# Performance work log

Hardware: AMD Instinct MI355X
Metric: run time of the kernel (lower is better)

The kernel has to match this reference:

```python
import jax, jax.numpy as jnp
import numpy as np

B, S, H, E, F, TOP_K = 4, 2048, 512, 16, 1024, 2


def setup_inputs() -> dict:
    key = jax.random.key(0)
    k0, k1, k2, k3, k4 = jax.random.split(key, 5)
    scale = 0.02
    return {
        "inputs": jax.random.normal(k0, (B, S, H), dtype=jnp.float32),
        "router_w": jax.random.normal(k1, (E, H), dtype=jnp.float32) * scale,
        "gate_w": jax.random.normal(k2, (E, H, F), dtype=jnp.float32) * scale,
        "up_w": jax.random.normal(k3, (E, H, F), dtype=jnp.float32) * scale,
        "down_w": jax.random.normal(k4, (E, F, H), dtype=jnp.float32) * scale,
    }


def _moe_forward(inputs, router_w, gate_w, up_w, down_w):
    b, s, h = inputs.shape
    x = inputs.reshape(-1, h)                      # [T, H]
    T = x.shape[0]
    # --- routing: topk of logits then fp32 softmax over the k selected ---
    router_logits = x @ router_w.T                 # [T, E]
    top_vals, top_idx = jax.lax.top_k(router_logits, TOP_K)   # [T, K]
    weights = jax.nn.softmax(top_vals.astype(jnp.float32), axis=-1)  # [T, K]
    # dense combine weights: w[t, e] = routing weight if expert e selected else 0
    combine = jnp.zeros((T, router_w.shape[0]), jnp.float32)
    combine = combine.at[jnp.arange(T)[:, None], top_idx].set(weights)  # [T, E]

    # --- per-expert SwiGLU MLP, weighted combine (scan over experts) ---
    def step(acc, ew):
        wg, wu, wd, ce = ew                        # [H,F], [H,F], [F,H], [T]
        hid = jax.nn.silu(x @ wg) * (x @ wu)       # [T, F]
        y = hid @ wd                               # [T, H]
        return acc + ce[:, None] * y, None

    out0 = jnp.zeros_like(x)
    out, _ = jax.lax.scan(step, out0, (gate_w, up_w, down_w, combine.T))
    return out.reshape(b, s, h), router_logits, top_idx


def reference(inputs, router_w, gate_w, up_w, down_w):
    out, router_logits, selected_experts = _moe_forward(
        inputs, router_w, gate_w, up_w, down_w)
    return out
```

## Files before the change

kernel.cpp:

```cpp
#include <hip/hip_runtime.h>
#include <cstdint>
#include <cstddef>

#define T_TOK 8192
#define H_DIM 512
#define E_NUM 16
#define F_DIM 1024

typedef __bf16 bf16x8 __attribute__((ext_vector_type(8)));
typedef float f32x4 __attribute__((ext_vector_type(4)));

#define OFF_XBF  0UL
#define OFF_HID  8388608UL
#define OFF_GW   41943040UL
#define OFF_UW   58720256UL
#define OFF_DW   75497472UL
#define OFF_STOK 92274688UL
#define OFF_SW   92340224UL
#define OFF_TOPE 92405760UL
#define OFF_TOPW 92471296UL
#define OFF_CNT  92536832UL
#define OFF_CUR  92537856UL
#define OFF_OFFS 92538880UL
#define OFF_SIDX 92539904UL
#define OFF_L128 92605440UL
#define OFF_L64  92606464UL
#define OFF_YB   OFF_GW

__device__ __forceinline__ unsigned short f2bf(float f) {
  union { float f; uint32_t u; } v; v.f = f;
  uint32_t r = v.u + 0x7fffu + ((v.u >> 16) & 1u);
  return (unsigned short)(r >> 16);
}

__device__ __forceinline__ float bf2f(unsigned short u) {
  union { uint32_t u; float f; } v; v.u = (uint32_t)u << 16;
  return v.f;
}

__device__ __forceinline__ void gld16(const void* g, void* l) {
  __builtin_amdgcn_global_load_lds(
      (const __attribute__((address_space(1))) unsigned int*)g,
      (__attribute__((address_space(3))) unsigned int*)l, 16, 0, 0);
}

__device__ __forceinline__ uint4 pack8(const float4 v[8], int i) {
  uint4 q;
  q.x = (uint32_t)f2bf(((const float*)&v[0])[i]) | ((uint32_t)f2bf(((const float*)&v[1])[i]) << 16);
  q.y = (uint32_t)f2bf(((const float*)&v[2])[i]) | ((uint32_t)f2bf(((const float*)&v[3])[i]) << 16);
  q.z = (uint32_t)f2bf(((const float*)&v[4])[i]) | ((uint32_t)f2bf(((const float*)&v[5])[i]) << 16);
  q.w = (uint32_t)f2bf(((const float*)&v[6])[i]) | ((uint32_t)f2bf(((const float*)&v[7])[i]) << 16);
  return q;
}

__global__ __launch_bounds__(256) void k_pre(
    const float* __restrict__ x, const float* __restrict__ rw,
    const float* __restrict__ gw, const float* __restrict__ uw,
    unsigned short* __restrict__ xbf, int* __restrict__ tope,
    float* __restrict__ topw,
    unsigned short* __restrict__ gws, unsigned short* __restrict__ uws,
    int* __restrict__ counts) {
  const int bid = blockIdx.x;
  const int tid = threadIdx.x;
  __shared__ int lh[E_NUM];

  if (bid < 2048) {
    const int e = bid >> 7, mat = (bid >> 6) & 1, kc = (bid >> 2) & 15, f2 = bid & 3;
    const float* src = (mat ? uw : gw) + (size_t)e * H_DIM * F_DIM
                     + (size_t)kc * 32 * F_DIM + f2 * 256;
    unsigned short* dst = mat ? uws : gws;
    const int nb = tid & 63, kb = tid >> 6;
    const float* s0 = src + (size_t)kb * 8 * F_DIM + nb * 4;
    float4 v[8];
    #pragma unroll
    for (int j = 0; j < 8; ++j) v[j] = *(const float4*)(s0 + (size_t)j * F_DIM);
    #pragma unroll
    for (int i = 0; i < 4; ++i) {
      const int nl = nb * 4 + i;
      const int fx = f2 * 2 + (nl >> 7), fi = nl & 127;
      const size_t ob = (((size_t)e * 8 + fx) * 16 + kc) * 4096;
      *(uint4*)&dst[ob + fi * 32 + ((kb ^ fi) & 3) * 8] = pack8(v, i);
    }
  } else {
    if (tid < E_NUM) lh[tid] = 0;
    __syncthreads();
    const int rb = bid - 2048;
    const int wave = tid >> 6, lane = tid & 63;
    const int t = rb * 4 + wave;
    const float4* xr = (const float4*)(x + (size_t)t * H_DIM + lane * 8);
    float4 a = xr[0], b = xr[1];
    float xi[8] = {a.x, a.y, a.z, a.w, b.x, b.y, b.z, b.w};
    uint4 o;
    o.x = (uint32_t)f2bf(xi[0]) | ((uint32_t)f2bf(xi[1]) << 16);
    o.y = (uint32_t)f2bf(xi[2]) | ((uint32_t)f2bf(xi[3]) << 16);
    o.z = (uint32_t)f2bf(xi[4]) | ((uint32_t)f2bf(xi[5]) << 16);
    o.w = (uint32_t)f2bf(xi[6]) | ((uint32_t)f2bf(xi[7]) << 16);
    *(uint4*)(xbf + (size_t)t * H_DIM + lane * 8) = o;
    float acc[E_NUM];
    #pragma unroll
    for (int e = 0; e < E_NUM; ++e) {
      const float4* wr = (const float4*)(rw + e * H_DIM + lane * 8);
      float4 wa = wr[0], wb = wr[1];
      acc[e] = xi[0]*wa.x + xi[1]*wa.y + xi[2]*wa.z + xi[3]*wa.w
             + xi[4]*wb.x + xi[5]*wb.y + xi[6]*wb.z + xi[7]*wb.w;
    }
    #pragma unroll
    for (int off = 1; off < 64; off <<= 1) {
      #pragma unroll
      for (int e = 0; e < E_NUM; ++e) acc[e] += __shfl_xor(acc[e], off);
    }
    if (lane == 0) {
      int e0 = 0; float v0 = acc[0];
      #pragma unroll
      for (int e = 1; e < E_NUM; ++e) if (acc[e] > v0) { v0 = acc[e]; e0 = e; }
      int e1 = -1; float v1 = -3.4e38f;
      #pragma unroll
      for (int e = 0; e < E_NUM; ++e) if (e != e0 && acc[e] > v1) { v1 = acc[e]; e1 = e; }
      float ee = __expf(v1 - v0);
      float inv = 1.0f / (1.0f + ee);
      tope[t*2]   = e0; tope[t*2+1] = e1;
      topw[t*2]   = inv; topw[t*2+1] = ee * inv;
      atomicAdd(&lh[e0], 1);
      atomicAdd(&lh[e1], 1);
    }
    __syncthreads();
    if (tid < E_NUM && lh[tid] > 0) atomicAdd(&counts[tid * 16], lh[tid]);
  }
}

__global__ void k_offsets(const int* __restrict__ counts, int* __restrict__ offs,
                          int* __restrict__ list128, int* __restrict__ list64) {
  __shared__ int sc[16], b128[16], b64[16];
  if (threadIdx.x == 0) {
    int s = 0, a = 0, b = 0;
    for (int e = 0; e < E_NUM; ++e) {
      int c = counts[e * 16];
      sc[e] = c; b128[e] = a; b64[e] = b;
      offs[e] = s;
      s += c; a += (c + 127) >> 7; b += (c + 63) >> 6;
    }
    offs[16] = s; offs[18] = a; offs[19] = b;
  }
  __syncthreads();
  for (int e = 0; e < E_NUM; ++e) {
    const int n1 = (sc[e] + 127) >> 7;
    for (int ti = threadIdx.x; ti < n1; ti += 64) list128[b128[e] + ti] = (e << 24) | (ti << 7);
    const int n2 = (sc[e] + 63) >> 6;
    for (int ti = threadIdx.x; ti < n2; ti += 64) list64[b64[e] + ti] = (e << 24) | (ti << 6);
  }
}

__global__ __launch_bounds__(256) void k_scatter(
    const int* __restrict__ tope, const float* __restrict__ topw,
    const int* __restrict__ offs, int* __restrict__ cursors,
    int* __restrict__ stok, float* __restrict__ sw, int* __restrict__ sidx) {
  __shared__ int lh[E_NUM];
  __shared__ int lbase[E_NUM];
  const int tid = threadIdx.x;
  const int t = blockIdx.x * 256 + tid;
  if (tid < E_NUM) lh[tid] = 0;
  __syncthreads();
  int e0 = tope[t*2], e1 = tope[t*2+1];
  int r0 = atomicAdd(&lh[e0], 1);
  int r1 = atomicAdd(&lh[e1], 1);
  __syncthreads();
  if (tid < E_NUM) lbase[tid] = atomicAdd(&cursors[tid * 16], lh[tid]);
  __syncthreads();
  int s0 = offs[e0] + lbase[e0] + r0;
  int s1 = offs[e1] + lbase[e1] + r1;
  stok[s0] = t; sw[s0] = topw[t*2];
  stok[s1] = t; sw[s1] = topw[t*2+1];
  sidx[t*2] = s0; sidx[t*2+1] = s1;
}

__global__ __launch_bounds__(256, 2) void k_gateup(
    const unsigned short* __restrict__ xbf,
    const unsigned short* __restrict__ gws, const unsigned short* __restrict__ uws,
    const int* __restrict__ stok, const int* __restrict__ counts,
    const int* __restrict__ offs, const int* __restrict__ list128,
    unsigned short* __restrict__ hid,
    const float* __restrict__ dwf, unsigned short* __restrict__ dws) {
  const int y = blockIdx.y;
  const int tid = threadIdx.x;

  if (y >= 160) {
    const int u = (y - 160) * 8 + blockIdx.x;
    const int e = u >> 6, kc = (u >> 1) & 31, ht = u & 1;
    const float* src = dwf + (size_t)e * F_DIM * H_DIM
                     + (size_t)kc * 32 * H_DIM + ht * 256;
    const int nb = tid & 63, kb = tid >> 6;
    const float* s0 = src + (size_t)kb * 8 * H_DIM + nb * 4;
    float4 v[8];
    #pragma unroll
    for (int j = 0; j < 8; ++j) v[j] = *(const float4*)(s0 + (size_t)j * H_DIM);
    const size_t ob = (((size_t)e * 2 + ht) * 32 + kc) * 8192;
    #pragma unroll
    for (int i = 0; i < 4; ++i) {
      const int n = nb * 4 + i;
      *(uint4*)&dws[ob + n * 32 + ((kb ^ n) & 3) * 8] = pack8(v, i);
    }
    return;
  }
  if (y >= offs[18]) return;
  const int v = list128[y];
  const int e = v >> 24, t0 = v & 0xffffff;
  const int cnt = counts[e * 16];
  const int base = offs[e];
  const int fx = blockIdx.x;

  __shared__ __align__(16) unsigned short sb[2][3][4096];

  const int wave = tid >> 6, lane = tid & 63;
  const int l15 = lane & 15, hi = lane >> 4;
  const int wm = wave >> 1, wn = wave & 1;

  const int r0 = tid >> 2, slot = tid & 3;
  const int rr0 = min(t0 + r0, cnt - 1), rr1 = min(t0 + r0 + 64, cnt - 1);
  const char* sA0 = (const char*)xbf + (size_t)stok[base + rr0] * 1024 + ((slot ^ (r0 & 3)) * 16);
  const char* sA1 = (const char*)xbf + (size_t)stok[base + rr1] * 1024 + ((slot ^ (r0 & 3)) * 16);
  const char* sG = (const char*)gws + (((size_t)e * 8 + fx) * 16) * 8192 + tid * 16;
  const char* sU = (const char*)uws + (((size_t)e * 8 + fx) * 16) * 8192 + tid * 16;
  unsigned short* const dA = &sb[0][0][wave * 512];
  unsigned short* const dG = &sb[0][1][wave * 512];
  unsigned short* const dU = &sb[0][2][wave * 512];
  const int bufo = 3 * 4096;

  f32x4 accg[4][4] = {}; f32x4 accu[4][4] = {};

  #define STAGE_GU(b, kk) { \
    gld16(sA0 + (kk)*64, dA + (b)*bufo); \
    gld16(sA1 + (kk)*64, dA + (b)*bufo + 2048); \
    gld16(sG + (size_t)(kk)*8192, dG + (b)*bufo); \
    gld16(sG + (size_t)(kk)*8192 + 4096, dG + (b)*bufo + 2048); \
    gld16(sU + (size_t)(kk)*8192, dU + (b)*bufo); \
    gld16(sU + (size_t)(kk)*8192 + 4096, dU + (b)*bufo + 2048); }

  STAGE_GU(0, 0);
  __syncthreads();
  #pragma unroll 1
  for (int kk = 0; kk < 16; ++kk) {
    const int cur = kk & 1;
    if (kk < 15) STAGE_GU(cur ^ 1, kk + 1);
    const unsigned short* lA = &sb[cur][0][0];
    const unsigned short* lG = &sb[cur][1][0];
    const unsigned short* lU = &sb[cur][2][0];
    bf16x8 a[4], bg[4], bu[4];
    #pragma unroll
    for (int m = 0; m < 4; ++m) {
      int row = wm*64 + m*16 + l15;
      a[m] = *(const bf16x8*)((const char*)lA + row*64 + (((hi ^ row) & 3) << 4));
    }
    #pragma unroll
    for (int s = 0; s < 4; ++s) {
      int row = wn*64 + s*16 + l15;
      int o = row*64 + (((hi ^ row) & 3) << 4);
      bg[s] = *(const bf16x8*)((const char*)lG + o);
      bu[s] = *(const bf16x8*)((const char*)lU + o);
    }
    #pragma unroll
    for (int m = 0; m < 4; ++m)
      #pragma unroll
      for (int s = 0; s < 4; ++s) {
        accg[m][s] = __builtin_amdgcn_mfma_f32_16x16x32_bf16(a[m], bg[s], accg[m][s], 0, 0, 0);
        accu[m][s] = __builtin_amdgcn_mfma_f32_16x16x32_bf16(a[m], bu[s], accu[m][s], 0, 0, 0);
      }
    __syncthreads();
  }
  #undef STAGE_GU

  #pragma unroll
  for (int m = 0; m < 4; ++m)
    #pragma unroll
    for (int r = 0; r < 4; ++r) {
      int row = t0 + wm*64 + m*16 + hi*4 + r;
      if (row < cnt) {
        #pragma unroll
        for (int s = 0; s < 4; ++s) {
          float g = accg[m][s][r], u = accu[m][s][r];
          float h = g / (1.0f + __expf(-g)) * u;
          hid[(size_t)(base + row) * 1024 + fx*128 + wn*64 + s*16 + l15] = f2bf(h);
        }
      }
    }
}

__global__ __launch_bounds__(256, 3) void k_down(
    const unsigned short* __restrict__ hid, const unsigned short* __restrict__ dws,
    const int* __restrict__ counts, const int* __restrict__ offs,
    const int* __restrict__ list64, unsigned short* __restrict__ ybuf) {
  const int y = blockIdx.y;
  if (y >= offs[19]) return;
  const int v = list64[y];
  const int e = v >> 24, t0 = v & 0xffffff;
  const int cnt = counts[e * 16];
  const int base = offs[e];
  const int ht = blockIdx.x;

  __shared__ __align__(16) unsigned short sbA[2][2048];
  __shared__ __align__(16) unsigned short sbW[2][8192];

  const int tid = threadIdx.x;
  const int wave = tid >> 6, lane = tid & 63;
  const int l15 = lane & 15, hi = lane >> 4;

  const int r0 = tid >> 2, slot = tid & 3;
  const int rr = min(t0 + r0, cnt - 1);
  const char* sA = (const char*)hid + (size_t)(base + rr) * 2048 + ((slot ^ (r0 & 3)) * 16);
  const char* sW = (const char*)dws + (((size_t)e * 2 + ht) * 32) * 16384 + tid * 16;
  unsigned short* const dA = &sbA[0][wave * 512];
  unsigned short* const dW = &sbW[0][wave * 512];

  f32x4 acc[4][4] = {};

  #define STAGE_DN(b, kk) { \
    gld16(sA + (kk)*64, dA + (b)*2048); \
    const char* w = sW + (size_t)(kk)*16384; \
    gld16(w,         dW + (b)*8192); \
    gld16(w + 4096,  dW + (b)*8192 + 2048); \
    gld16(w + 8192,  dW + (b)*8192 + 4096); \
    gld16(w + 12288, dW + (b)*8192 + 6144); }

  STAGE_DN(0, 0);
  __syncthreads();
  #pragma unroll 1
  for (int kk = 0; kk < 32; ++kk) {
    const int cur = kk & 1;
    if (kk < 31) STAGE_DN(cur ^ 1, kk + 1);
    const unsigned short* lA = &sbA[cur][0];
    const unsigned short* lW = &sbW[cur][0];
    bf16x8 a[4], b[4];
    #pragma unroll
    for (int m = 0; m < 4; ++m) {
      int row = m*16 + l15;
      a[m] = *(const bf16x8*)((const char*)lA + row*64 + (((hi ^ row) & 3) << 4));
    }
    #pragma unroll
    for (int s = 0; s < 4; ++s) {
      int row = wave*64 + s*16 + l15;
      b[s] = *(const bf16x8*)((const char*)lW + row*64 + (((hi ^ row) & 3) << 4));
    }
    #pragma unroll
    for (int m = 0; m < 4; ++m)
      #pragma unroll
      for (int s = 0; s < 4; ++s)
        acc[m][s] = __builtin_amdgcn_mfma_f32_16x16x32_bf16(a[m], b[s], acc[m][s], 0, 0, 0);
    __syncthreads();
  }
  #undef STAGE_DN

  #pragma unroll
  for (int m = 0; m < 4; ++m)
    #pragma unroll
    for (int r = 0; r < 4; ++r) {
      int row = t0 + m*16 + hi*4 + r;
      if (row < cnt) {
        unsigned short* yy = ybuf + (size_t)(base + row) * 512 + ht*256 + wave*64;
        #pragma unroll
        for (int s = 0; s < 4; ++s)
          yy[s*16 + l15] = f2bf(acc[m][s][r]);
      }
    }
}

__global__ __launch_bounds__(256) void k_gather(
    const unsigned short* __restrict__ ybuf, const int* __restrict__ sidx,
    const float* __restrict__ topw, float* __restrict__ out) {
  const int wave = threadIdx.x >> 6, lane = threadIdx.x & 63;
  const int t = blockIdx.x * 4 + wave;
  const int s0 = sidx[t*2], s1 = sidx[t*2+1];
  const float w0 = topw[t*2], w1 = topw[t*2+1];
  uint4 a = *(const uint4*)(ybuf + (size_t)s0 * 512 + lane * 8);
  uint4 b = *(const uint4*)(ybuf + (size_t)s1 * 512 + lane * 8);
  float4 o0, o1;
  o0.x = w0*bf2f((unsigned short)(a.x)) + w1*bf2f((unsigned short)(b.x));
  o0.y = w0*bf2f((unsigned short)(a.x>>16)) + w1*bf2f((unsigned short)(b.x>>16));
  o0.z = w0*bf2f((unsigned short)(a.y)) + w1*bf2f((unsigned short)(b.y));
  o0.w = w0*bf2f((unsigned short)(a.y>>16)) + w1*bf2f((unsigned short)(b.y>>16));
  o1.x = w0*bf2f((unsigned short)(a.z)) + w1*bf2f((unsigned short)(b.z));
  o1.y = w0*bf2f((unsigned short)(a.z>>16)) + w1*bf2f((unsigned short)(b.z>>16));
  o1.z = w0*bf2f((unsigned short)(a.w)) + w1*bf2f((unsigned short)(b.w));
  o1.w = w0*bf2f((unsigned short)(a.w>>16)) + w1*bf2f((unsigned short)(b.w>>16));
  float* orow = out + (size_t)t * H_DIM + lane * 8;
  *(float4*)orow = o0;
  *(float4*)(orow + 4) = o1;
}

extern "C" void kernel_launch(void* const* d_in, const int* in_sizes, int n_in,
                              void* d_out, int out_size, void* d_ws, size_t ws_size,
                              hipStream_t stream) {
  const float* x  = (const float*)d_in[0];
  const float* rw = (const float*)d_in[1];
  const float* gw = (const float*)d_in[2];
  const float* uw = (const float*)d_in[3];
  const float* dw = (const float*)d_in[4];
  float* out = (float*)d_out;
  char* ws = (char*)d_ws;

  unsigned short* xbf = (unsigned short*)(ws + OFF_XBF);
  unsigned short* hid = (unsigned short*)(ws + OFF_HID);
  unsigned short* gws = (unsigned short*)(ws + OFF_GW);
  unsigned short* uws = (unsigned short*)(ws + OFF_UW);
  unsigned short* dws = (unsigned short*)(ws + OFF_DW);
  unsigned short* ybuf = (unsigned short*)(ws + OFF_YB);
  int*   stok    = (int*)(ws + OFF_STOK);
  float* swt     = (float*)(ws + OFF_SW);
  int*   tope    = (int*)(ws + OFF_TOPE);
  float* topw    = (float*)(ws + OFF_TOPW);
  int*   counts  = (int*)(ws + OFF_CNT);
  int*   cursors = (int*)(ws + OFF_CUR);
  int*   offs    = (int*)(ws + OFF_OFFS);
  int*   sidx    = (int*)(ws + OFF_SIDX);
  int*   list128 = (int*)(ws + OFF_L128);
  int*   list64  = (int*)(ws + OFF_L64);

  hipMemsetAsync(ws + OFF_CNT, 0, 2048 + 128, stream);

  k_pre<<<4096, 256, 0, stream>>>(x, rw, gw, uw, xbf, tope, topw, gws, uws, counts);
  k_offsets<<<1, 64, 0, stream>>>(counts, offs, list128, list64);
  k_scatter<<<T_TOK / 256, 256, 0, stream>>>(tope, topw, offs, cursors, stok, swt, sidx);
  k_gateup<<<dim3(8, 288), 256, 0, stream>>>(
      xbf, gws, uws, stok, counts, offs, list128, hid, dw, dws);
  k_down<<<dim3(2, 288), 256, 0, stream>>>(
      hid, dws, counts, offs, list64, ybuf);
  k_gather<<<T_TOK / 4, 256, 0, stream>>>(ybuf, sidx, topw, out);
}
```

Baseline: 157.3 us.

## Triple-buffer gate/up and down GEMM loads; move down-weight conversion to preprocessing kernel

Both grouped GEMM kernels move from double-buffered to triple-buffered LDS staging. They prefetch two k-steps ahead and use explicit vmcnt waits instead of __syncthreads, so global loads stay in flight across iterations. The down-weight fp32-to-bf16 conversion moves out of k_gateup into k_pre, which shrinks the gate/up grid. k_down's occupancy hint drops from 3 to 2 blocks per CU to make room for the larger shared memory, trading occupancy for deeper prefetch.

```diff
diff --git a/kernel.cpp b/kernel.cpp
--- a/kernel.cpp
+++ b/kernel.cpp
@@ -56,10 +56,11 @@
 __global__ __launch_bounds__(256) void k_pre(
     const float* __restrict__ x, const float* __restrict__ rw,
     const float* __restrict__ gw, const float* __restrict__ uw,
+    const float* __restrict__ dw,
     unsigned short* __restrict__ xbf, int* __restrict__ tope,
     float* __restrict__ topw,
     unsigned short* __restrict__ gws, unsigned short* __restrict__ uws,
-    int* __restrict__ counts) {
+    unsigned short* __restrict__ dws, int* __restrict__ counts) {
   const int bid = blockIdx.x;
   const int tid = threadIdx.x;
   __shared__ int lh[E_NUM];
@@ -81,10 +82,25 @@
       const size_t ob = (((size_t)e * 8 + fx) * 16 + kc) * 4096;
       *(uint4*)&dst[ob + fi * 32 + ((kb ^ fi) & 3) * 8] = pack8(v, i);
     }
+  } else if (bid < 3072) {
+    const int u = bid - 2048;
+    const int e = u >> 6, kc = (u >> 1) & 31, ht = u & 1;
+    const float* src = dw + (size_t)e * F_DIM * H_DIM + (size_t)kc * 32 * H_DIM + ht * 256;
+    const int nb = tid & 63, kb = tid >> 6;
+    const float* s0 = src + (size_t)kb * 8 * H_DIM + nb * 4;
+    float4 v[8];
+    #pragma unroll
+    for (int j = 0; j < 8; ++j) v[j] = *(const float4*)(s0 + (size_t)j * H_DIM);
+    const size_t ob = (((size_t)e * 2 + ht) * 32 + kc) * 8192;
+    #pragma unroll
+    for (int i = 0; i < 4; ++i) {
+      const int n = nb * 4 + i;
+      *(uint4*)&dws[ob + n * 32 + ((kb ^ n) & 3) * 8] = pack8(v, i);
+    }
   } else {
     if (tid < E_NUM) lh[tid] = 0;
     __syncthreads();
-    const int rb = bid - 2048;
+    const int rb = bid - 3072;
     const int wave = tid >> 6, lane = tid & 63;
     const int t = rb * 4 + wave;
     const float4* xr = (const float4*)(x + (size_t)t * H_DIM + lane * 8);
@@ -178,29 +194,8 @@
     const unsigned short* __restrict__ gws, const unsigned short* __restrict__ uws,
     const int* __restrict__ stok, const int* __restrict__ counts,
     const int* __restrict__ offs, const int* __restrict__ list128,
-    unsigned short* __restrict__ hid,
-    const float* __restrict__ dwf, unsigned short* __restrict__ dws) {
+    unsigned short* __restrict__ hid) {
   const int y = blockIdx.y;
-  const int tid = threadIdx.x;
-
-  if (y >= 160) {
-    const int u = (y - 160) * 8 + blockIdx.x;
-    const int e = u >> 6, kc = (u >> 1) & 31, ht = u & 1;
-    const float* src = dwf + (size_t)e * F_DIM * H_DIM
-                     + (size_t)kc * 32 * H_DIM + ht * 256;
-    const int nb = tid & 63, kb = tid >> 6;
-    const float* s0 = src + (size_t)kb * 8 * H_DIM + nb * 4;
-    float4 v[8];
-    #pragma unroll
-    for (int j = 0; j < 8; ++j) v[j] = *(const float4*)(s0 + (size_t)j * H_DIM);
-    const size_t ob = (((size_t)e * 2 + ht) * 32 + kc) * 8192;
-    #pragma unroll
-    for (int i = 0; i < 4; ++i) {
-      const int n = nb * 4 + i;
-      *(uint4*)&dws[ob + n * 32 + ((kb ^ n) & 3) * 8] = pack8(v, i);
-    }
-    return;
-  }
   if (y >= offs[18]) return;
   const int v = list128[y];
   const int e = v >> 24, t0 = v & 0xffffff;
@@ -208,8 +203,9 @@
   const int base = offs[e];
   const int fx = blockIdx.x;
 
-  __shared__ __align__(16) unsigned short sb[2][3][4096];
-
+  __shared__ __align__(16) unsigned short sb[3][3][4096];
+
+  const int tid = threadIdx.x;
   const int wave = tid >> 6, lane = tid & 63;
   const int l15 = lane & 15, hi = lane >> 4;
   const int wm = wave >> 1, wn = wave & 1;
@@ -235,37 +231,43 @@
     gld16(sU + (size_t)(kk)*8192, dU + (b)*bufo); \
     gld16(sU + (size_t)(kk)*8192 + 4096, dU + (b)*bufo + 2048); }
 
+  #define GU_CHUNK(kk, DO_STAGE, VM) { \
+    if (DO_STAGE) STAGE_GU(b2, (kk) + 2); \
+    asm volatile("s_waitcnt vmcnt(" VM ") lgkmcnt(0)\n\ts_barrier" ::: "memory"); \
+    const unsigned short* lA = &sb[b0][0][0]; \
+    const unsigned short* lG = &sb[b0][1][0]; \
+    const unsigned short* lU = &sb[b0][2][0]; \
+    bf16x8 a[4], bg[4], bu[4]; \
+    _Pragma("unroll") \
+    for (int m = 0; m < 4; ++m) { \
+      int row = wm*64 + m*16 + l15; \
+      a[m] = *(const bf16x8*)((const char*)lA + row*64 + (((hi ^ row) & 3) << 4)); \
+    } \
+    _Pragma("unroll") \
+    for (int s = 0; s < 4; ++s) { \
+      int row = wn*64 + s*16 + l15; \
+      int o = row*64 + (((hi ^ row) & 3) << 4); \
+      bg[s] = *(const bf16x8*)((const char*)lG + o); \
+      bu[s] = *(const bf16x8*)((const char*)lU + o); \
+    } \
+    _Pragma("unroll") \
+    for (int m = 0; m < 4; ++m) \
+      _Pragma("unroll") \
+      for (int s = 0; s < 4; ++s) { \
+        accg[m][s] = __builtin_amdgcn_mfma_f32_16x16x32_bf16(a[m], bg[s], accg[m][s], 0, 0, 0); \
+        accu[m][s] = __builtin_amdgcn_mfma_f32_16x16x32_bf16(a[m], bu[s], accu[m][s], 0, 0, 0); \
+      } \
+    asm volatile("s_waitcnt lgkmcnt(0)\n\ts_barrier" ::: "memory"); \
+    int _t = b0; b0 = b1; b1 = b2; b2 = _t; }
+
+  int b0 = 0, b1 = 1, b2 = 2;
   STAGE_GU(0, 0);
-  __syncthreads();
+  STAGE_GU(1, 1);
   #pragma unroll 1
-  for (int kk = 0; kk < 16; ++kk) {
-    const int cur = kk & 1;
-    if (kk < 15) STAGE_GU(cur ^ 1, kk + 1);
-    const unsigned short* lA = &sb[cur][0][0];
-    const unsigned short* lG = &sb[cur][1][0];
-    const unsigned short* lU = &sb[cur][2][0];
-    bf16x8 a[4], bg[4], bu[4];
-    #pragma unroll
-    for (int m = 0; m < 4; ++m) {
-      int row = wm*64 + m*16 + l15;
-      a[m] = *(const bf16x8*)((const char*)lA + row*64 + (((hi ^ row) & 3) << 4));
-    }
-    #pragma unroll
-    for (int s = 0; s < 4; ++s) {
-      int row = wn*64 + s*16 + l15;
-      int o = row*64 + (((hi ^ row) & 3) << 4);
-      bg[s] = *(const bf16x8*)((const char*)lG + o);
-      bu[s] = *(const bf16x8*)((const char*)lU + o);
-    }
-    #pragma unroll
-    for (int m = 0; m < 4; ++m)
-      #pragma unroll
-      for (int s = 0; s < 4; ++s) {
-        accg[m][s] = __builtin_amdgcn_mfma_f32_16x16x32_bf16(a[m], bg[s], accg[m][s], 0, 0, 0);
-        accu[m][s] = __builtin_amdgcn_mfma_f32_16x16x32_bf16(a[m], bu[s], accu[m][s], 0, 0, 0);
-      }
-    __syncthreads();
-  }
+  for (int kk = 0; kk < 14; ++kk) GU_CHUNK(kk, 1, "12");
+  GU_CHUNK(14, 0, "6");
+  GU_CHUNK(15, 0, "0");
+  #undef GU_CHUNK
   #undef STAGE_GU
 
   #pragma unroll
@@ -284,7 +286,7 @@
     }
 }
 
-__global__ __launch_bounds__(256, 3) void k_down(
+__global__ __launch_bounds__(256, 2) void k_down(
     const unsigned short* __restrict__ hid, const unsigned short* __restrict__ dws,
     const int* __restrict__ counts, const int* __restrict__ offs,
     const int* __restrict__ list64, unsigned short* __restrict__ ybuf) {
@@ -296,8 +298,8 @@
   const int base = offs[e];
   const int ht = blockIdx.x;
 
-  __shared__ __align__(16) unsigned short sbA[2][2048];
-  __shared__ __align__(16) unsigned short sbW[2][8192];
+  __shared__ __align__(16) unsigned short sbA[3][2048];
+  __shared__ __align__(16) unsigned short sbW[3][8192];
 
   const int tid = threadIdx.x;
   const int wave = tid >> 6, lane = tid & 63;
@@ -320,32 +322,38 @@
     gld16(w + 8192,  dW + (b)*8192 + 4096); \
     gld16(w + 12288, dW + (b)*8192 + 6144); }
 
+  #define DN_CHUNK(kk, DO_STAGE, VM) { \
+    if (DO_STAGE) STAGE_DN(b2, (kk) + 2); \
+    asm volatile("s_waitcnt vmcnt(" VM ") lgkmcnt(0)\n\ts_barrier" ::: "memory"); \
+    const unsigned short* lA = &sbA[b0][0]; \
+    const unsigned short* lW = &sbW[b0][0]; \
+    bf16x8 a[4], b[4]; \
+    _Pragma("unroll") \
+    for (int m = 0; m < 4; ++m) { \
+      int row = m*16 + l15; \
+      a[m] = *(const bf16x8*)((const char*)lA + row*64 + (((hi ^ row) & 3) << 4)); \
+    } \
+    _Pragma("unroll") \
+    for (int s = 0; s < 4; ++s) { \
+      int row = wave*64 + s*16 + l15; \
+      b[s] = *(const bf16x8*)((const char*)lW + row*64 + (((hi ^ row) & 3) << 4)); \
+    } \
+    _Pragma("unroll") \
+    for (int m = 0; m < 4; ++m) \
+      _Pragma("unroll") \
+      for (int s = 0; s < 4; ++s) \
+        acc[m][s] = __builtin_amdgcn_mfma_f32_16x16x32_bf16(a[m], b[s], acc[m][s], 0, 0, 0); \
+    asm volatile("s_waitcnt lgkmcnt(0)\n\ts_barrier" ::: "memory"); \
+    int _t = b0; b0 = b1; b1 = b2; b2 = _t; }
+
+  int b0 = 0, b1 = 1, b2 = 2;
   STAGE_DN(0, 0);
-  __syncthreads();
+  STAGE_DN(1, 1);
   #pragma unroll 1
-  for (int kk = 0; kk < 32; ++kk) {
-    const int cur = kk & 1;
-    if (kk < 31) STAGE_DN(cur ^ 1, kk + 1);
-    const unsigned short* lA = &sbA[cur][0];
-    const unsigned short* lW = &sbW[cur][0];
-    bf16x8 a[4], b[4];
-    #pragma unroll
-    for (int m = 0; m < 4; ++m) {
-      int row = m*16 + l15;
-      a[m] = *(const bf16x8*)((const char*)lA + row*64 + (((hi ^ row) & 3) << 4));
-    }
-    #pragma unroll
-    for (int s = 0; s < 4; ++s) {
-      int row = wave*64 + s*16 + l15;
-      b[s] = *(const bf16x8*)((const char*)lW + row*64 + (((hi ^ row) & 3) << 4));
-    }
-    #pragma unroll
-    for (int m = 0; m < 4; ++m)
-      #pragma unroll
-      for (int s = 0; s < 4; ++s)
-        acc[m][s] = __builtin_amdgcn_mfma_f32_16x16x32_bf16(a[m], b[s], acc[m][s], 0, 0, 0);
-    __syncthreads();
-  }
+  for (int kk = 0; kk < 30; ++kk) DN_CHUNK(kk, 1, "10");
+  DN_CHUNK(30, 0, "5");
+  DN_CHUNK(31, 0, "0");
+  #undef DN_CHUNK
   #undef STAGE_DN
 
   #pragma unroll
@@ -415,11 +423,11 @@
 
   hipMemsetAsync(ws + OFF_CNT, 0, 2048 + 128, stream);
 
-  k_pre<<<4096, 256, 0, stream>>>(x, rw, gw, uw, xbf, tope, topw, gws, uws, counts);
+  k_pre<<<5120, 256, 0, stream>>>(x, rw, gw, uw, dw, xbf, tope, topw, gws, uws, dws, counts);
   k_offsets<<<1, 64, 0, stream>>>(counts, offs, list128, list64);
   k_scatter<<<T_TOK / 256, 256, 0, stream>>>(tope, topw, offs, cursors, stok, swt, sidx);
-  k_gateup<<<dim3(8, 288), 256, 0, stream>>>(
-      xbf, gws, uws, stok, counts, offs, list128, hid, dw, dws);
+  k_gateup<<<dim3(8, 160), 256, 0, stream>>>(
+      xbf, gws, uws, stok, counts, offs, list128, hid);
   k_down<<<dim3(2, 288), 256, 0, stream>>>(
       hid, dws, counts, offs, list64, ybuf);
   k_gather<<<T_TOK / 4, 256, 0, stream>>>(ybuf, sidx, topw, out);
```

Result: slower. 174.7 us (+11.1%).

## Move down-weight conversion into pre kernel and raise occupancy bounds

Applied to the files above, without the earlier changes.

The fp32-to-bf16 conversion and swizzle of the down-projection weights moves out of the gate/up kernel's extra grid rows and into the pre kernel. Each conversion block now handles two column halves, which halves the block count for the gate/up and down weight conversion. The gate/up grid shrinks to the GEMM rows only, and the launch-bound occupancy hints rise to 3 for gate/up and 4 for down. The aim is less dead grid and fewer branches in the GEMM kernel, plus more waves per CU, at the cost of tighter register budgets that could cause spills.

```diff
diff --git a/kernel.cpp b/kernel.cpp
--- a/kernel.cpp
+++ b/kernel.cpp
@@ -56,35 +56,61 @@
 __global__ __launch_bounds__(256) void k_pre(
     const float* __restrict__ x, const float* __restrict__ rw,
     const float* __restrict__ gw, const float* __restrict__ uw,
+    const float* __restrict__ dw,
     unsigned short* __restrict__ xbf, int* __restrict__ tope,
     float* __restrict__ topw,
     unsigned short* __restrict__ gws, unsigned short* __restrict__ uws,
-    int* __restrict__ counts) {
+    unsigned short* __restrict__ dws, int* __restrict__ counts) {
   const int bid = blockIdx.x;
   const int tid = threadIdx.x;
   __shared__ int lh[E_NUM];
 
-  if (bid < 2048) {
-    const int e = bid >> 7, mat = (bid >> 6) & 1, kc = (bid >> 2) & 15, f2 = bid & 3;
+  if (bid < 1024) {
+    const int e = bid >> 6, mat = (bid >> 5) & 1, kc = (bid >> 1) & 15, f2p = bid & 1;
     const float* src = (mat ? uw : gw) + (size_t)e * H_DIM * F_DIM
-                     + (size_t)kc * 32 * F_DIM + f2 * 256;
+                     + (size_t)kc * 32 * F_DIM + f2p * 512;
     unsigned short* dst = mat ? uws : gws;
     const int nb = tid & 63, kb = tid >> 6;
     const float* s0 = src + (size_t)kb * 8 * F_DIM + nb * 4;
-    float4 v[8];
-    #pragma unroll
-    for (int j = 0; j < 8; ++j) v[j] = *(const float4*)(s0 + (size_t)j * F_DIM);
+    float4 va[8], vb[8];
+    #pragma unroll
+    for (int j = 0; j < 8; ++j) va[j] = *(const float4*)(s0 + (size_t)j * F_DIM);
+    #pragma unroll
+    for (int j = 0; j < 8; ++j) vb[j] = *(const float4*)(s0 + (size_t)j * F_DIM + 256);
     #pragma unroll
     for (int i = 0; i < 4; ++i) {
       const int nl = nb * 4 + i;
-      const int fx = f2 * 2 + (nl >> 7), fi = nl & 127;
-      const size_t ob = (((size_t)e * 8 + fx) * 16 + kc) * 4096;
-      *(uint4*)&dst[ob + fi * 32 + ((kb ^ fi) & 3) * 8] = pack8(v, i);
+      const int fi = nl & 127;
+      const int fxa = f2p * 4 + (nl >> 7);
+      const size_t oba = (((size_t)e * 8 + fxa) * 16 + kc) * 4096;
+      *(uint4*)&dst[oba + fi * 32 + ((kb ^ fi) & 3) * 8] = pack8(va, i);
+      const int fxb = fxa + 2;
+      const size_t obb = (((size_t)e * 8 + fxb) * 16 + kc) * 4096;
+      *(uint4*)&dst[obb + fi * 32 + ((kb ^ fi) & 3) * 8] = pack8(vb, i);
+    }
+  } else if (bid < 1536) {
+    const int u = bid - 1024;
+    const int e = u >> 5, kc = u & 31;
+    const float* src = dw + (size_t)e * F_DIM * H_DIM + (size_t)kc * 32 * H_DIM;
+    const int nb = tid & 63, kb = tid >> 6;
+    const float* s0 = src + (size_t)kb * 8 * H_DIM + nb * 4;
+    float4 va[8], vb[8];
+    #pragma unroll
+    for (int j = 0; j < 8; ++j) va[j] = *(const float4*)(s0 + (size_t)j * H_DIM);
+    #pragma unroll
+    for (int j = 0; j < 8; ++j) vb[j] = *(const float4*)(s0 + (size_t)j * H_DIM + 256);
+    const size_t oba = (((size_t)e * 2 + 0) * 32 + kc) * 8192;
+    const size_t obb = (((size_t)e * 2 + 1) * 32 + kc) * 8192;
+    #pragma unroll
+    for (int i = 0; i < 4; ++i) {
+      const int n = nb * 4 + i;
+      *(uint4*)&dws[oba + n * 32 + ((kb ^ n) & 3) * 8] = pack8(va, i);
+      *(uint4*)&dws[obb + n * 32 + ((kb ^ n) & 3) * 8] = pack8(vb, i);
     }
   } else {
     if (tid < E_NUM) lh[tid] = 0;
     __syncthreads();
-    const int rb = bid - 2048;
+    const int rb = bid - 1536;
     const int wave = tid >> 6, lane = tid & 63;
     const int t = rb * 4 + wave;
     const float4* xr = (const float4*)(x + (size_t)t * H_DIM + lane * 8);
@@ -173,34 +199,13 @@
   sidx[t*2] = s0; sidx[t*2+1] = s1;
 }
 
-__global__ __launch_bounds__(256, 2) void k_gateup(
+__global__ __launch_bounds__(256, 3) void k_gateup(
     const unsigned short* __restrict__ xbf,
     const unsigned short* __restrict__ gws, const unsigned short* __restrict__ uws,
     const int* __restrict__ stok, const int* __restrict__ counts,
     const int* __restrict__ offs, const int* __restrict__ list128,
-    unsigned short* __restrict__ hid,
-    const float* __restrict__ dwf, unsigned short* __restrict__ dws) {
+    unsigned short* __restrict__ hid) {
   const int y = blockIdx.y;
-  const int tid = threadIdx.x;
-
-  if (y >= 160) {
-    const int u = (y - 160) * 8 + blockIdx.x;
-    const int e = u >> 6, kc = (u >> 1) & 31, ht = u & 1;
-    const float* src = dwf + (size_t)e * F_DIM * H_DIM
-                     + (size_t)kc * 32 * H_DIM + ht * 256;
-    const int nb = tid & 63, kb = tid >> 6;
-    const float* s0 = src + (size_t)kb * 8 * H_DIM + nb * 4;
-    float4 v[8];
-    #pragma unroll
-    for (int j = 0; j < 8; ++j) v[j] = *(const float4*)(s0 + (size_t)j * H_DIM);
-    const size_t ob = (((size_t)e * 2 + ht) * 32 + kc) * 8192;
-    #pragma unroll
-    for (int i = 0; i < 4; ++i) {
-      const int n = nb * 4 + i;
-      *(uint4*)&dws[ob + n * 32 + ((kb ^ n) & 3) * 8] = pack8(v, i);
-    }
-    return;
-  }
   if (y >= offs[18]) return;
   const int v = list128[y];
   const int e = v >> 24, t0 = v & 0xffffff;
@@ -210,6 +215,7 @@
 
   __shared__ __align__(16) unsigned short sb[2][3][4096];
 
+  const int tid = threadIdx.x;
   const int wave = tid >> 6, lane = tid & 63;
   const int l15 = lane & 15, hi = lane >> 4;
   const int wm = wave >> 1, wn = wave & 1;
@@ -284,7 +290,7 @@
     }
 }
 
-__global__ __launch_bounds__(256, 3) void k_down(
+__global__ __launch_bounds__(256, 4) void k_down(
     const unsigned short* __restrict__ hid, const unsigned short* __restrict__ dws,
     const int* __restrict__ counts, const int* __restrict__ offs,
     const int* __restrict__ list64, unsigned short* __restrict__ ybuf) {
@@ -415,11 +421,11 @@
 
   hipMemsetAsync(ws + OFF_CNT, 0, 2048 + 128, stream);
 
-  k_pre<<<4096, 256, 0, stream>>>(x, rw, gw, uw, xbf, tope, topw, gws, uws, counts);
+  k_pre<<<3584, 256, 0, stream>>>(x, rw, gw, uw, dw, xbf, tope, topw, gws, uws, dws, counts);
   k_offsets<<<1, 64, 0, stream>>>(counts, offs, list128, list64);
   k_scatter<<<T_TOK / 256, 256, 0, stream>>>(tope, topw, offs, cursors, stok, swt, sidx);
-  k_gateup<<<dim3(8, 288), 256, 0, stream>>>(
-      xbf, gws, uws, stok, counts, offs, list128, hid, dw, dws);
+  k_gateup<<<dim3(8, 160), 256, 0, stream>>>(
+      xbf, gws, uws, stok, counts, offs, list128, hid);
   k_down<<<dim3(2, 288), 256, 0, stream>>>(
       hid, dws, counts, offs, list64, ybuf);
   k_gather<<<T_TOK / 4, 256, 0, stream>>>(ybuf, sidx, topw, out);
```

After: 181.1 us. +15.2%, slower.

## Stage gate/up weight conversion through LDS and schedule down-weight conversion blocks first

Applied to the files above, without the earlier changes.

The gate/up weight bf16 conversion in k_pre now writes packed rows into a swizzled shared-memory buffer, then each thread reads back four 16-byte chunks for one output row. This makes the global stores contiguous instead of scattered across rows. In k_gateup, the down-weight conversion blocks move from the end of the grid (y>=160) to the start (y<128), so they get scheduled ahead of the GEMM blocks. The cost is an extra 16KB of LDS and a barrier in k_pre.

```diff
diff --git a/kernel.cpp b/kernel.cpp
--- a/kernel.cpp
+++ b/kernel.cpp
@@ -44,7 +44,7 @@
       (__attribute__((address_space(3))) unsigned int*)l, 16, 0, 0);
 }
 
-__device__ __forceinline__ uint4 pack8(const float4 v[8], int i) {
+__device__ __forceinline__ uint4 pack8f(const float4 v[8], int i) {
   uint4 q;
   q.x = (uint32_t)f2bf(((const float*)&v[0])[i]) | ((uint32_t)f2bf(((const float*)&v[1])[i]) << 16);
   q.y = (uint32_t)f2bf(((const float*)&v[2])[i]) | ((uint32_t)f2bf(((const float*)&v[3])[i]) << 16);
@@ -62,6 +62,7 @@
     int* __restrict__ counts) {
   const int bid = blockIdx.x;
   const int tid = threadIdx.x;
+  __shared__ __align__(16) uint32_t lsu[4096];
   __shared__ int lh[E_NUM];
 
   if (bid < 2048) {
@@ -69,6 +70,7 @@
     const float* src = (mat ? uw : gw) + (size_t)e * H_DIM * F_DIM
                      + (size_t)kc * 32 * F_DIM + f2 * 256;
     unsigned short* dst = mat ? uws : gws;
+    const size_t obase0 = (((size_t)e * 8 + f2 * 2) * 16 + kc) * 4096;
     const int nb = tid & 63, kb = tid >> 6;
     const float* s0 = src + (size_t)kb * 8 * F_DIM + nb * 4;
     float4 v[8];
@@ -76,10 +78,21 @@
     for (int j = 0; j < 8; ++j) v[j] = *(const float4*)(s0 + (size_t)j * F_DIM);
     #pragma unroll
     for (int i = 0; i < 4; ++i) {
-      const int nl = nb * 4 + i;
-      const int fx = f2 * 2 + (nl >> 7), fi = nl & 127;
-      const size_t ob = (((size_t)e * 8 + fx) * 16 + kc) * 4096;
-      *(uint4*)&dst[ob + fi * 32 + ((kb ^ fi) & 3) * 8] = pack8(v, i);
+      const int n = nb * 4 + i;
+      const int jr = n >> 1, sw = (jr ^ (jr >> 3)) & 7;
+      const int ccs = (((n & 1) << 2) + kb) ^ sw;
+      *(uint4*)&lsu[jr * 32 + ccs * 4] = pack8f(v, i);
+    }
+    __syncthreads();
+    const int n = tid;
+    const int jr = n >> 1, sw = (jr ^ (jr >> 3)) & 7;
+    #pragma unroll
+    for (int c = 0; c < 4; ++c) {
+      const int ccs = (((n & 1) << 2) + c) ^ sw;
+      uint4 q = *(const uint4*)&lsu[jr * 32 + ccs * 4];
+      const int fi = n & 127, s = (c ^ fi) & 3;
+      const size_t ob = obase0 + (size_t)(n >> 7) * 16 * 4096;
+      *(uint4*)&dst[ob + fi * 32 + s * 8] = q;
     }
   } else {
     if (tid < E_NUM) lh[tid] = 0;
@@ -180,11 +193,11 @@
     const int* __restrict__ offs, const int* __restrict__ list128,
     unsigned short* __restrict__ hid,
     const float* __restrict__ dwf, unsigned short* __restrict__ dws) {
-  const int y = blockIdx.y;
   const int tid = threadIdx.x;
-
-  if (y >= 160) {
-    const int u = (y - 160) * 8 + blockIdx.x;
+  const int yy = blockIdx.y;
+
+  if (yy < 128) {
+    const int u = yy * 8 + blockIdx.x;
     const int e = u >> 6, kc = (u >> 1) & 31, ht = u & 1;
     const float* src = dwf + (size_t)e * F_DIM * H_DIM
                      + (size_t)kc * 32 * H_DIM + ht * 256;
@@ -197,10 +210,12 @@
     #pragma unroll
     for (int i = 0; i < 4; ++i) {
       const int n = nb * 4 + i;
-      *(uint4*)&dws[ob + n * 32 + ((kb ^ n) & 3) * 8] = pack8(v, i);
+      *(uint4*)&dws[ob + n * 32 + ((kb ^ n) & 3) * 8] = pack8f(v, i);
     }
     return;
   }
+
+  const int y = yy - 128;
   if (y >= offs[18]) return;
   const int v = list128[y];
   const int e = v >> 24, t0 = v & 0xffffff;
```

Measured after the change: 161.8 us. 2.9% more time.
